# Performance work log

Hardware: AMD Instinct MI355X
Metric: run time of the kernel (lower is better)

Reference implementation:

```python
import jax, jax.numpy as jnp
import numpy as np

N = 8192
IN_F = 256
OUT_F = 64
ALPHA = 0.2  # LeakyReLU negative slope
NEG_INF = -9e15


def setup_inputs() -> dict:
    key = jax.random.key(0)
    k1, k2, k3, k4 = jax.random.split(key, 4)
    input_h = jax.random.normal(k1, (N, IN_F), dtype=jnp.float32)
    # xavier_normal with gain=1.414 ~ std = 1.414*sqrt(2/(fan_in+fan_out))
    W = jax.random.normal(k2, (IN_F, OUT_F), dtype=jnp.float32) * (1.414 * np.sqrt(2.0 / (IN_F + OUT_F)))
    a = jax.random.normal(k3, (2 * OUT_F, 1), dtype=jnp.float32) * (1.414 * np.sqrt(2.0 / (2 * OUT_F + 1)))
    adj = jax.random.randint(k4, (N, N), 0, 2).astype(jnp.int32)
    return {"input_h": input_h, "adj": adj, "W": W, "a": a}


def reference(input_h, adj, W, a):
    # h = X @ W : [N, OUT_F]
    h = input_h @ W
    # Pairwise concat score: a^T [h_i || h_j] == (h_i @ a1) + (h_j @ a2)
    a1 = a[:OUT_F]   # [OUT_F, 1]
    a2 = a[OUT_F:]   # [OUT_F, 1]
    f1 = h @ a1      # [N, 1] -> contribution of source node i
    f2 = h @ a2      # [N, 1] -> contribution of target node j
    e = jax.nn.leaky_relu(f1 + f2.T, negative_slope=ALPHA)  # [N, N]
    # Masked softmax over neighbors (adj > 0), dropout is identity in eval mode
    attention = jax.nn.softmax(jnp.where(adj > 0, e, NEG_INF), axis=-1)
    h_prime = attention @ h  # [N, OUT_F]
    # concat=True -> ELU activation
    return jax.nn.elu(h_prime)
```

## Files before the change

kernel.cpp:

```cpp
#include <hip/hip_runtime.h>
#include <hip/hip_bf16.h>


using short8 = __attribute__((ext_vector_type(8))) short;
using f32x4  = __attribute__((ext_vector_type(4))) float;

#define NN     8192
#define INF_   256
#define OUTF   64
#define LR_A   0.2f
#define LOG2E  1.4426950408889634f
#define ROWS   16
#define TILE_C 256
#define CQW    2048
#define NTILES (CQW / TILE_C)
#define ROWB   1040

__device__ __forceinline__ unsigned short f2bf_rne(float x) {
  unsigned int u = __float_as_uint(x);
  u += 0x7FFFu + ((u >> 16) & 1u);
  return (unsigned short)(u >> 16);
}

__global__ __launch_bounds__(256) void gat_pre(
    const float* __restrict__ input, const float* __restrict__ W,
    const float* __restrict__ a, unsigned short* __restrict__ hp,
    float* __restrict__ f1, float* __restrict__ f2) {
  __shared__ float WT[OUTF][260];
  int tid = threadIdx.x;
  for (int idx = tid; idx < INF_ * OUTF; idx += 256) {
    int c = idx >> 6, f = idx & 63;
    WT[f][c] = W[idx];
  }
  __syncthreads();
  int w = tid >> 6, l = tid & 63;
  int i0 = blockIdx.x * 16 + w * 4;
  const float4* r0 = (const float4*)(input + (long)(i0 + 0) * INF_);
  const float4* r1 = (const float4*)(input + (long)(i0 + 1) * INF_);
  const float4* r2 = (const float4*)(input + (long)(i0 + 2) * INF_);
  const float4* r3 = (const float4*)(input + (long)(i0 + 3) * INF_);
  float h0 = 0.f, h1 = 0.f, h2 = 0.f, h3 = 0.f;
#pragma unroll 4
  for (int c4 = 0; c4 < INF_ / 4; ++c4) {
    float4 wv = *(const float4*)&WT[l][c4 * 4];
    float4 v0 = r0[c4], v1 = r1[c4], v2 = r2[c4], v3 = r3[c4];
    h0 = fmaf(v0.x, wv.x, h0); h0 = fmaf(v0.y, wv.y, h0);
    h0 = fmaf(v0.z, wv.z, h0); h0 = fmaf(v0.w, wv.w, h0);
    h1 = fmaf(v1.x, wv.x, h1); h1 = fmaf(v1.y, wv.y, h1);
    h1 = fmaf(v1.z, wv.z, h1); h1 = fmaf(v1.w, wv.w, h1);
    h2 = fmaf(v2.x, wv.x, h2); h2 = fmaf(v2.y, wv.y, h2);
    h2 = fmaf(v2.z, wv.z, h2); h2 = fmaf(v2.w, wv.w, h2);
    h3 = fmaf(v3.x, wv.x, h3); h3 = fmaf(v3.y, wv.y, h3);
    h3 = fmaf(v3.z, wv.z, h3); h3 = fmaf(v3.w, wv.w, h3);
  }
  float a1k = a[l], a2k = a[OUTF + l];
  float hh[4] = {h0, h1, h2, h3};
#pragma unroll
  for (int r = 0; r < 4; ++r) {
    int i = i0 + r;
    float t1 = hh[r] * a1k, t2 = hh[r] * a2k;
#pragma unroll
    for (int off = 32; off; off >>= 1) {
      t1 += __shfl_xor(t1, off);
      t2 += __shfl_xor(t2, off);
    }
    int gran = (((i >> 5) * 4) + (l >> 4)) * 64 + ((i >> 3) & 3) * 16 + (l & 15);
    hp[(long)gran * 8 + (i & 7)] = f2bf_rne(hh[r]);
    if (l == 0) { f1[i] = t1 * LOG2E; f2[i] = t2 * LOG2E; }
  }
}

__global__ __launch_bounds__(256, 4) void gat_main(
    const int* __restrict__ adj, const unsigned short* __restrict__ hp,
    const float* __restrict__ f1, const float* __restrict__ f2,
    float* __restrict__ numP, float* __restrict__ denP) {
  __shared__ __align__(16) char um[2 * ROWS * ROWB];
  __shared__ float ssum[4][ROWS];
  __shared__ float f1s[ROWS], shifts[ROWS], red[4];
  int tid = threadIdx.x;
  int w = tid >> 6, l = tid & 63;
  int i0 = blockIdx.x * ROWS;
  int cq = blockIdx.y;

  float fm = -1e30f;
  for (int jj = tid * 4; jj < NN; jj += 256 * 4) {
    float4 v = *(const float4*)(f2 + jj);
    fm = fmaxf(fm, fmaxf(fmaxf(v.x, v.y), fmaxf(v.z, v.w)));
  }
#pragma unroll
  for (int off = 32; off; off >>= 1) fm = fmaxf(fm, __shfl_xor(fm, off));
  if (l == 0) red[w] = fm;
  __syncthreads();
  if (tid == 0) {
    float m = fmaxf(fmaxf(red[0], red[1]), fmaxf(red[2], red[3]));
    red[0] = m;
  }
  __syncthreads();
  float Fmax = red[0];
  if (tid < ROWS) {
    float v = f1[i0 + tid];
    f1s[tid] = v;
    float s = v + Fmax;
    shifts[tid] = fmaxf(s, LR_A * s);
  }
  __syncthreads();

  int q = l & 15, g = l >> 4;
  float f1r = f1s[q], sh = shifts[q];
  float u1 = f1r - sh;
  float u2 = LR_A * f1r - sh;
  f32x4 acc0 = {0.f, 0.f, 0.f, 0.f}, acc1 = acc0, acc2 = acc0, acc3 = acc0;
  float srow = 0.f;

  const int* adjb = adj + (long)cq * CQW;

  auto stage = [&](int t, int b) {
#pragma unroll
    for (int k = 0; k < 4; ++k) {
      int r = w * 4 + k;
      const int* src = adjb + (long)(i0 + r) * NN + t * TILE_C + l * 4;
      char* d = um + b * (ROWS * ROWB) + r * ROWB;
      __builtin_amdgcn_global_load_lds(
          (const __attribute__((address_space(1))) void*)src,
          (__attribute__((address_space(3))) void*)d, 16, 0, 0);
    }
  };

  stage(0, 0);
  __syncthreads();

  for (int t = 0; t < NTILES; ++t) {
    int b = t & 1;
    if (t + 1 < NTILES) stage(t + 1, b ^ 1);

    const char* base = um + b * (ROWS * ROWB) + q * ROWB;
#pragma unroll
    for (int s = 0; s < 2; ++s) {
      int koff = w * 256 + s * 128 + g * 32;
      int4 A0 = *(const int4*)(base + koff);
      int4 A1 = *(const int4*)(base + koff + 16);
      int jb = cq * CQW + t * TILE_C + w * 64 + s * 32 + g * 8;
      float4 F0 = *(const float4*)(f2 + jb);
      float4 F1 = *(const float4*)(f2 + jb + 4);
      float fa[8] = {F0.x, F0.y, F0.z, F0.w, F1.x, F1.y, F1.z, F1.w};
      int   aa[8] = {A0.x, A0.y, A0.z, A0.w, A1.x, A1.y, A1.z, A1.w};

      union { short8 v; unsigned short u[8]; } pa;
      float ps = 0.f;
#pragma unroll
      for (int e = 0; e < 8; ++e) {
        float arg = fmaxf(u1 + fa[e], fmaf(LR_A, fa[e], u2));
        float pe = (aa[e] > 0) ? exp2f(arg) : 0.f;
        ps += pe;
        pa.u[e] = f2bf_rne(pe);
      }
      srow += ps;

      int K32 = cq * 64 + t * 8 + w * 2 + s;
      const unsigned short* hb = hp + (long)K32 * 4 * 64 * 8 + l * 8;
      short8 b0 = *(const short8*)(hb + 0 * 64 * 8);
      short8 b1 = *(const short8*)(hb + 1 * 64 * 8);
      short8 b2 = *(const short8*)(hb + 2 * 64 * 8);
      short8 b3 = *(const short8*)(hb + 3 * 64 * 8);
      acc0 = __builtin_amdgcn_mfma_f32_16x16x32_bf16(pa.v, b0, acc0, 0, 0, 0);
      acc1 = __builtin_amdgcn_mfma_f32_16x16x32_bf16(pa.v, b1, acc1, 0, 0, 0);
      acc2 = __builtin_amdgcn_mfma_f32_16x16x32_bf16(pa.v, b2, acc2, 0, 0, 0);
      acc3 = __builtin_amdgcn_mfma_f32_16x16x32_bf16(pa.v, b3, acc3, 0, 0, 0);
    }
    __syncthreads();
  }

  srow += __shfl_xor(srow, 16);
  srow += __shfl_xor(srow, 32);
  if (l < ROWS) ssum[w][l] = srow;

  float* accs = (float*)um;
#pragma unroll
  for (int r = 0; r < 4; ++r) {
    accs[(w * ROWS + g * 4 + r) * OUTF + 0 * 16 + q] = acc0[r];
    accs[(w * ROWS + g * 4 + r) * OUTF + 1 * 16 + q] = acc1[r];
    accs[(w * ROWS + g * 4 + r) * OUTF + 2 * 16 + q] = acc2[r];
    accs[(w * ROWS + g * 4 + r) * OUTF + 3 * 16 + q] = acc3[r];
  }
  __syncthreads();

  for (int idx = tid; idx < ROWS * OUTF; idx += 256) {
    int m = idx >> 6, n = idx & 63;
    float num = 0.f, den = 0.f;
#pragma unroll
    for (int ww = 0; ww < 4; ++ww) {
      num += accs[(ww * ROWS + m) * OUTF + n];
      den += ssum[ww][m];
    }
    numP[((long)cq * NN + i0 + m) * OUTF + n] = num;
    if (n == 0) denP[(long)cq * NN + i0 + m] = den;
  }
}

__global__ __launch_bounds__(256) void gat_fin(
    const float* __restrict__ numP, const float* __restrict__ denP,
    float* __restrict__ out) {
  int gid = blockIdx.x * 256 + threadIdx.x;
  int row = gid >> 6, n = gid & 63;
  float num = 0.f, den = 0.f;
#pragma unroll
  for (int c = 0; c < 4; ++c) {
    num += numP[((long)c * NN + row) * OUTF + n];
    den += denP[(long)c * NN + row];
  }
  float v = num / den;
  out[gid] = v > 0.f ? v : expm1f(v);
}

extern "C" void kernel_launch(void* const* d_in, const int* in_sizes, int n_in,
                              void* d_out, int out_size, void* d_ws, size_t ws_size,
                              hipStream_t stream) {
  const float* input = (const float*)d_in[0];
  const int*   adj   = (const int*)d_in[1];
  const float* W     = (const float*)d_in[2];
  const float* a     = (const float*)d_in[3];
  float* out = (float*)d_out;
  char* ws = (char*)d_ws;
  unsigned short* hp = (unsigned short*)ws;
  float* f1   = (float*)(ws + (1 << 20));
  float* f2   = (float*)(ws + (1 << 20) + (32 << 10));
  float* numP = (float*)(ws + (1 << 20) + (64 << 10));
  float* denP = (float*)(ws + (1 << 20) + (64 << 10) + (8 << 20));
  (void)in_sizes; (void)n_in; (void)out_size; (void)ws_size;

  gat_pre<<<512, 256, 0, stream>>>(input, W, a, hp, f1, f2);
  gat_main<<<dim3(512, 4), 256, 0, stream>>>(adj, hp, f1, f2, numP, denP);
  gat_fin<<<NN * OUTF / 256, 256, 0, stream>>>(numP, denP, out);
}
```

Measured before the change: 100.2 us.

## Stage adj and h tiles through LDS with a deeper async pipeline

Rebuilds the main loop's memory pipeline. Adjacency tiles now go through a three-slot LDS ring with XOR swizzling to avoid bank conflicts. The bf16 h tiles are prefetched into double-buffered LDS instead of being read directly from global memory, and the f2 slice is cached in shared memory. Explicit vmcnt waits plus raw barriers replace the per-tile __syncthreads. Tile width is halved and launch bounds drop to 2 blocks per SIMD to fit the larger LDS footprint, which cuts occupancy and makes correctness depend on the hand-counted waitcnt.

```diff
diff --git a/kernel.cpp b/kernel.cpp
--- a/kernel.cpp
+++ b/kernel.cpp
@@ -11,10 +11,11 @@
 #define LR_A   0.2f
 #define LOG2E  1.4426950408889634f
 #define ROWS   16
-#define TILE_C 256
+#define TILE_C 128
 #define CQW    2048
 #define NTILES (CQW / TILE_C)
-#define ROWB   1040
+#define ADJSLOT 8192
+#define HPSLOT  16384
 
 __device__ __forceinline__ unsigned short f2bf_rne(float x) {
   unsigned int u = __float_as_uint(x);
@@ -70,11 +71,13 @@
   }
 }
 
-__global__ __launch_bounds__(256, 4) void gat_main(
+__global__ __launch_bounds__(256, 2) void gat_main(
     const int* __restrict__ adj, const unsigned short* __restrict__ hp,
     const float* __restrict__ f1, const float* __restrict__ f2,
     float* __restrict__ numP, float* __restrict__ denP) {
-  __shared__ __align__(16) char um[2 * ROWS * ROWB];
+  __shared__ __align__(16) char adjS[3 * ADJSLOT];
+  __shared__ __align__(16) char hpS[2 * HPSLOT];
+  __shared__ float f2s[CQW];
   __shared__ float ssum[4][ROWS];
   __shared__ float f1s[ROWS], shifts[ROWS], red[4];
   int tid = threadIdx.x;
@@ -83,18 +86,17 @@
   int cq = blockIdx.y;
 
   float fm = -1e30f;
-  for (int jj = tid * 4; jj < NN; jj += 256 * 4) {
+  for (int jj = tid * 4; jj < NN; jj += 1024) {
     float4 v = *(const float4*)(f2 + jj);
     fm = fmaxf(fm, fmaxf(fmaxf(v.x, v.y), fmaxf(v.z, v.w)));
   }
+  for (int jj = tid * 4; jj < CQW; jj += 1024)
+    *(float4*)&f2s[jj] = *(const float4*)(f2 + cq * CQW + jj);
 #pragma unroll
   for (int off = 32; off; off >>= 1) fm = fmaxf(fm, __shfl_xor(fm, off));
   if (l == 0) red[w] = fm;
   __syncthreads();
-  if (tid == 0) {
-    float m = fmaxf(fmaxf(red[0], red[1]), fmaxf(red[2], red[3]));
-    red[0] = m;
-  }
+  if (tid == 0) red[0] = fmaxf(fmaxf(red[0], red[1]), fmaxf(red[2], red[3]));
   __syncthreads();
   float Fmax = red[0];
   if (tid < ROWS) {
@@ -107,74 +109,88 @@
 
   int q = l & 15, g = l >> 4;
   float f1r = f1s[q], sh = shifts[q];
-  float u1 = f1r - sh;
-  float u2 = LR_A * f1r - sh;
+  float u1 = f1r - sh, u2 = LR_A * f1r - sh;
   f32x4 acc0 = {0.f, 0.f, 0.f, 0.f}, acc1 = acc0, acc2 = acc0, acc3 = acc0;
   float srow = 0.f;
 
-  const int* adjb = adj + (long)cq * CQW;
-
-  auto stage = [&](int t, int b) {
-#pragma unroll
-    for (int k = 0; k < 4; ++k) {
-      int r = w * 4 + k;
-      const int* src = adjb + (long)(i0 + r) * NN + t * TILE_C + l * 4;
-      char* d = um + b * (ROWS * ROWB) + r * ROWB;
+  auto stage_adj = [&](int t, int slot) {
+#pragma unroll
+    for (int j = 0; j < 2; ++j) {
+      int rr = w * 4 + j * 2 + (l >> 5);
+      const int* src = adj + (long)(i0 + rr) * NN + cq * CQW + t * TILE_C
+                       + (((l & 31) ^ (rr & 7)) << 2);
+      char* d = adjS + slot * ADJSLOT + (w * 4 + j * 2) * 512;
       __builtin_amdgcn_global_load_lds(
           (const __attribute__((address_space(1))) void*)src,
           (__attribute__((address_space(3))) void*)d, 16, 0, 0);
     }
   };
-
-  stage(0, 0);
-  __syncthreads();
+  auto stage_hp = [&](int t, int slot) {
+    const unsigned short* base = hp + (long)(cq * 64 + t * 4 + w) * 2048 + l * 8;
+#pragma unroll
+    for (int j = 0; j < 4; ++j) {
+      const unsigned short* src = base + j * 512;
+      char* d = hpS + slot * HPSLOT + w * 4096 + j * 1024;
+      __builtin_amdgcn_global_load_lds(
+          (const __attribute__((address_space(1))) void*)src,
+          (__attribute__((address_space(3))) void*)d, 16, 0, 0);
+    }
+  };
+
+  stage_hp(0, 0);
+  stage_adj(0, 0);
+  stage_adj(1, 1);
 
   for (int t = 0; t < NTILES; ++t) {
-    int b = t & 1;
-    if (t + 1 < NTILES) stage(t + 1, b ^ 1);
-
-    const char* base = um + b * (ROWS * ROWB) + q * ROWB;
-#pragma unroll
-    for (int s = 0; s < 2; ++s) {
-      int koff = w * 256 + s * 128 + g * 32;
-      int4 A0 = *(const int4*)(base + koff);
-      int4 A1 = *(const int4*)(base + koff + 16);
-      int jb = cq * CQW + t * TILE_C + w * 64 + s * 32 + g * 8;
-      float4 F0 = *(const float4*)(f2 + jb);
-      float4 F1 = *(const float4*)(f2 + jb + 4);
-      float fa[8] = {F0.x, F0.y, F0.z, F0.w, F1.x, F1.y, F1.z, F1.w};
-      int   aa[8] = {A0.x, A0.y, A0.z, A0.w, A1.x, A1.y, A1.z, A1.w};
-
-      union { short8 v; unsigned short u[8]; } pa;
-      float ps = 0.f;
-#pragma unroll
-      for (int e = 0; e < 8; ++e) {
-        float arg = fmaxf(u1 + fa[e], fmaf(LR_A, fa[e], u2));
-        float pe = (aa[e] > 0) ? exp2f(arg) : 0.f;
-        ps += pe;
-        pa.u[e] = f2bf_rne(pe);
-      }
-      srow += ps;
-
-      int K32 = cq * 64 + t * 8 + w * 2 + s;
-      const unsigned short* hb = hp + (long)K32 * 4 * 64 * 8 + l * 8;
-      short8 b0 = *(const short8*)(hb + 0 * 64 * 8);
-      short8 b1 = *(const short8*)(hb + 1 * 64 * 8);
-      short8 b2 = *(const short8*)(hb + 2 * 64 * 8);
-      short8 b3 = *(const short8*)(hb + 3 * 64 * 8);
-      acc0 = __builtin_amdgcn_mfma_f32_16x16x32_bf16(pa.v, b0, acc0, 0, 0, 0);
-      acc1 = __builtin_amdgcn_mfma_f32_16x16x32_bf16(pa.v, b1, acc1, 0, 0, 0);
-      acc2 = __builtin_amdgcn_mfma_f32_16x16x32_bf16(pa.v, b2, acc2, 0, 0, 0);
-      acc3 = __builtin_amdgcn_mfma_f32_16x16x32_bf16(pa.v, b3, acc3, 0, 0, 0);
-    }
-    __syncthreads();
+    if (t < NTILES - 1) {
+      asm volatile("s_waitcnt vmcnt(2)" ::: "memory");
+    } else {
+      asm volatile("s_waitcnt vmcnt(0)" ::: "memory");
+    }
+    __builtin_amdgcn_s_barrier();
+    if (t + 1 < NTILES) stage_hp(t + 1, (t + 1) & 1);
+    if (t + 2 < NTILES) stage_adj(t + 2, (t + 2) % 3);
+
+    const char* ab = adjS + (t % 3) * ADJSLOT + q * 512;
+    int koff = w * 128 + g * 32;
+    int sw = (q & 7) << 4;
+    int4 A0 = *(const int4*)(ab + (koff ^ sw));
+    int4 A1 = *(const int4*)(ab + ((koff + 16) ^ sw));
+    const float* f2b = f2s + t * TILE_C + w * 32 + g * 8;
+    float4 F0 = *(const float4*)(f2b);
+    float4 F1 = *(const float4*)(f2b + 4);
+    float fa[8] = {F0.x, F0.y, F0.z, F0.w, F1.x, F1.y, F1.z, F1.w};
+    int   aa[8] = {A0.x, A0.y, A0.z, A0.w, A1.x, A1.y, A1.z, A1.w};
+
+    union { short8 v; unsigned short u[8]; } pa;
+    float ps = 0.f;
+#pragma unroll
+    for (int e = 0; e < 8; ++e) {
+      float arg = fmaxf(u1 + fa[e], fmaf(LR_A, fa[e], u2));
+      float pe = (aa[e] > 0) ? exp2f(arg) : 0.f;
+      ps += pe;
+      pa.u[e] = f2bf_rne(pe);
+    }
+    srow += ps;
+
+    const unsigned short* hb =
+        (const unsigned short*)(hpS + (t & 1) * HPSLOT + w * 4096) + l * 8;
+    short8 b0 = *(const short8*)(hb + 0 * 512);
+    short8 b1 = *(const short8*)(hb + 1 * 512);
+    short8 b2 = *(const short8*)(hb + 2 * 512);
+    short8 b3 = *(const short8*)(hb + 3 * 512);
+    acc0 = __builtin_amdgcn_mfma_f32_16x16x32_bf16(pa.v, b0, acc0, 0, 0, 0);
+    acc1 = __builtin_amdgcn_mfma_f32_16x16x32_bf16(pa.v, b1, acc1, 0, 0, 0);
+    acc2 = __builtin_amdgcn_mfma_f32_16x16x32_bf16(pa.v, b2, acc2, 0, 0, 0);
+    acc3 = __builtin_amdgcn_mfma_f32_16x16x32_bf16(pa.v, b3, acc3, 0, 0, 0);
   }
 
   srow += __shfl_xor(srow, 16);
   srow += __shfl_xor(srow, 32);
+
+  __syncthreads();
   if (l < ROWS) ssum[w][l] = srow;
-
-  float* accs = (float*)um;
+  float* accs = (float*)hpS;
 #pragma unroll
   for (int r = 0; r < 4; ++r) {
     accs[(w * ROWS + g * 4 + r) * OUTF + 0 * 16 + q] = acc0[r];
```

New measurement: 121.8 us. 1.22x slower.

## Replace LDS-staged adjacency tiles with register-prefetched direct loads and manual vmcnt pipeline

Applied to the files above, without the earlier changes.

Drops the double-buffered global-to-LDS staging of adjacency tiles and the per-tile block barriers. Each wave now loads its own adjacency and h fragments straight into registers several steps ahead, using explicit vmcnt waits and sched barriers in a fully unrolled 16-step loop. The f2 slice is cached in shared memory and occupancy hint drops from 4 to 3 waves per SIMD. This removes block-wide syncs and LDS round trips, but adds register pressure and depends on exact vmcnt counts being correct.

```diff
diff --git a/kernel.cpp b/kernel.cpp
--- a/kernel.cpp
+++ b/kernel.cpp
@@ -11,10 +11,7 @@
 #define LR_A   0.2f
 #define LOG2E  1.4426950408889634f
 #define ROWS   16
-#define TILE_C 256
 #define CQW    2048
-#define NTILES (CQW / TILE_C)
-#define ROWB   1040
 
 __device__ __forceinline__ unsigned short f2bf_rne(float x) {
   unsigned int u = __float_as_uint(x);
@@ -70,11 +67,12 @@
   }
 }
 
-__global__ __launch_bounds__(256, 4) void gat_main(
+__global__ __launch_bounds__(256, 3) void gat_main(
     const int* __restrict__ adj, const unsigned short* __restrict__ hp,
     const float* __restrict__ f1, const float* __restrict__ f2,
     float* __restrict__ numP, float* __restrict__ denP) {
-  __shared__ __align__(16) char um[2 * ROWS * ROWB];
+  __shared__ __align__(16) float umem[4 * ROWS * OUTF];
+  float* f2s = umem;
   __shared__ float ssum[4][ROWS];
   __shared__ float f1s[ROWS], shifts[ROWS], red[4];
   int tid = threadIdx.x;
@@ -83,18 +81,17 @@
   int cq = blockIdx.y;
 
   float fm = -1e30f;
-  for (int jj = tid * 4; jj < NN; jj += 256 * 4) {
+  for (int jj = tid * 4; jj < NN; jj += 1024) {
     float4 v = *(const float4*)(f2 + jj);
     fm = fmaxf(fm, fmaxf(fmaxf(v.x, v.y), fmaxf(v.z, v.w)));
   }
+  for (int jj = tid * 4; jj < CQW; jj += 1024)
+    *(float4*)&f2s[jj] = *(const float4*)(f2 + cq * CQW + jj);
 #pragma unroll
   for (int off = 32; off; off >>= 1) fm = fmaxf(fm, __shfl_xor(fm, off));
   if (l == 0) red[w] = fm;
   __syncthreads();
-  if (tid == 0) {
-    float m = fmaxf(fmaxf(red[0], red[1]), fmaxf(red[2], red[3]));
-    red[0] = m;
-  }
+  if (tid == 0) red[0] = fmaxf(fmaxf(red[0], red[1]), fmaxf(red[2], red[3]));
   __syncthreads();
   float Fmax = red[0];
   if (tid < ROWS) {
@@ -107,74 +104,85 @@
 
   int q = l & 15, g = l >> 4;
   float f1r = f1s[q], sh = shifts[q];
-  float u1 = f1r - sh;
-  float u2 = LR_A * f1r - sh;
+  float u1 = f1r - sh, u2 = LR_A * f1r - sh;
   f32x4 acc0 = {0.f, 0.f, 0.f, 0.f}, acc1 = acc0, acc2 = acc0, acc3 = acc0;
   float srow = 0.f;
 
-  const int* adjb = adj + (long)cq * CQW;
-
-  auto stage = [&](int t, int b) {
-#pragma unroll
-    for (int k = 0; k < 4; ++k) {
-      int r = w * 4 + k;
-      const int* src = adjb + (long)(i0 + r) * NN + t * TILE_C + l * 4;
-      char* d = um + b * (ROWS * ROWB) + r * ROWB;
-      __builtin_amdgcn_global_load_lds(
-          (const __attribute__((address_space(1))) void*)src,
-          (__attribute__((address_space(3))) void*)d, 16, 0, 0);
+  const int* adjw = adj + (long)(i0 + q) * NN + cq * CQW + w * 512 + g * 8;
+  const unsigned short* hpw = hp + (long)(cq * 64 + w * 16) * 2048 + l * 8;
+  const float* f2w = f2s + w * 512 + g * 8;
+
+  int4   aS[4][2];
+  short8 hS[2][4];
+
+#define IADJ(SLOT, T) { int _t = (T) < 16 ? (T) : 15;                        \
+    const int* _p = adjw + _t * 32;                                          \
+    aS[SLOT][0] = *(const int4*)_p; aS[SLOT][1] = *(const int4*)(_p + 4); }
+#define IHP(SLOT, T) { int _t = (T) < 16 ? (T) : 15;                         \
+    const unsigned short* _p = hpw + (long)_t * 2048;                        \
+    hS[SLOT][0] = *(const short8*)_p;                                        \
+    hS[SLOT][1] = *(const short8*)(_p + 512);                                \
+    hS[SLOT][2] = *(const short8*)(_p + 1024);                               \
+    hS[SLOT][3] = *(const short8*)(_p + 1536); }
+
+  auto compute = [&](const int4* A, const short8* H, int t) {
+    const float* fb = f2w + t * 32;
+    float4 F0 = *(const float4*)fb, F1 = *(const float4*)(fb + 4);
+    float fa[8] = {F0.x, F0.y, F0.z, F0.w, F1.x, F1.y, F1.z, F1.w};
+    int   aa[8] = {A[0].x, A[0].y, A[0].z, A[0].w,
+                   A[1].x, A[1].y, A[1].z, A[1].w};
+    union { short8 v; unsigned short u[8]; } pa;
+    float ps = 0.f;
+#pragma unroll
+    for (int e = 0; e < 8; ++e) {
+      float arg = fmaxf(u1 + fa[e], fmaf(LR_A, fa[e], u2));
+      float pe = (aa[e] > 0) ? exp2f(arg) : 0.f;
+      ps += pe;
+      pa.u[e] = f2bf_rne(pe);
     }
+    srow += ps;
+    acc0 = __builtin_amdgcn_mfma_f32_16x16x32_bf16(pa.v, H[0], acc0, 0, 0, 0);
+    acc1 = __builtin_amdgcn_mfma_f32_16x16x32_bf16(pa.v, H[1], acc1, 0, 0, 0);
+    acc2 = __builtin_amdgcn_mfma_f32_16x16x32_bf16(pa.v, H[2], acc2, 0, 0, 0);
+    acc3 = __builtin_amdgcn_mfma_f32_16x16x32_bf16(pa.v, H[3], acc3, 0, 0, 0);
   };
 
-  stage(0, 0);
-  __syncthreads();
-
-  for (int t = 0; t < NTILES; ++t) {
-    int b = t & 1;
-    if (t + 1 < NTILES) stage(t + 1, b ^ 1);
-
-    const char* base = um + b * (ROWS * ROWB) + q * ROWB;
-#pragma unroll
-    for (int s = 0; s < 2; ++s) {
-      int koff = w * 256 + s * 128 + g * 32;
-      int4 A0 = *(const int4*)(base + koff);
-      int4 A1 = *(const int4*)(base + koff + 16);
-      int jb = cq * CQW + t * TILE_C + w * 64 + s * 32 + g * 8;
-      float4 F0 = *(const float4*)(f2 + jb);
-      float4 F1 = *(const float4*)(f2 + jb + 4);
-      float fa[8] = {F0.x, F0.y, F0.z, F0.w, F1.x, F1.y, F1.z, F1.w};
-      int   aa[8] = {A0.x, A0.y, A0.z, A0.w, A1.x, A1.y, A1.z, A1.w};
-
-      union { short8 v; unsigned short u[8]; } pa;
-      float ps = 0.f;
-#pragma unroll
-      for (int e = 0; e < 8; ++e) {
-        float arg = fmaxf(u1 + fa[e], fmaf(LR_A, fa[e], u2));
-        float pe = (aa[e] > 0) ? exp2f(arg) : 0.f;
-        ps += pe;
-        pa.u[e] = f2bf_rne(pe);
-      }
-      srow += ps;
-
-      int K32 = cq * 64 + t * 8 + w * 2 + s;
-      const unsigned short* hb = hp + (long)K32 * 4 * 64 * 8 + l * 8;
-      short8 b0 = *(const short8*)(hb + 0 * 64 * 8);
-      short8 b1 = *(const short8*)(hb + 1 * 64 * 8);
-      short8 b2 = *(const short8*)(hb + 2 * 64 * 8);
-      short8 b3 = *(const short8*)(hb + 3 * 64 * 8);
-      acc0 = __builtin_amdgcn_mfma_f32_16x16x32_bf16(pa.v, b0, acc0, 0, 0, 0);
-      acc1 = __builtin_amdgcn_mfma_f32_16x16x32_bf16(pa.v, b1, acc1, 0, 0, 0);
-      acc2 = __builtin_amdgcn_mfma_f32_16x16x32_bf16(pa.v, b2, acc2, 0, 0, 0);
-      acc3 = __builtin_amdgcn_mfma_f32_16x16x32_bf16(pa.v, b3, acc3, 0, 0, 0);
-    }
-    __syncthreads();
-  }
+#define STEP(SLOT, HC, HN, T, VM)                                            \
+    IHP(HN, (T) + 1);                                                        \
+    IADJ(((SLOT) + 3) & 3, (T) + 3);                                         \
+    __builtin_amdgcn_sched_barrier(0);                                       \
+    asm volatile("s_waitcnt vmcnt(" VM ")" ::: "memory");                    \
+    __builtin_amdgcn_sched_barrier(0);                                       \
+    compute(aS[SLOT], hS[HC], T);
+
+  IADJ(0, 0) IADJ(1, 1) IADJ(2, 2) IHP(0, 0)
+
+  STEP(0, 0, 1,  0, "6")
+  STEP(1, 1, 0,  1, "8")
+  STEP(2, 0, 1,  2, "8")
+  STEP(3, 1, 0,  3, "8")
+  STEP(0, 0, 1,  4, "8")
+  STEP(1, 1, 0,  5, "8")
+  STEP(2, 0, 1,  6, "8")
+  STEP(3, 1, 0,  7, "8")
+  STEP(0, 0, 1,  8, "8")
+  STEP(1, 1, 0,  9, "8")
+  STEP(2, 0, 1, 10, "8")
+  STEP(3, 1, 0, 11, "8")
+  STEP(0, 0, 1, 12, "8")
+  STEP(1, 1, 0, 13, "8")
+  STEP(2, 0, 1, 14, "8")
+  STEP(3, 1, 0, 15, "8")
+#undef STEP
+#undef IADJ
+#undef IHP
 
   srow += __shfl_xor(srow, 16);
   srow += __shfl_xor(srow, 32);
+
+  __syncthreads();
   if (l < ROWS) ssum[w][l] = srow;
-
-  float* accs = (float*)um;
+  float* accs = umem;
 #pragma unroll
   for (int r = 0; r < 4; ++r) {
     accs[(w * ROWS + g * 4 + r) * OUTF + 0 * 16 + q] = acc0[r];
```

After: 143.6 us. +43.3%, slower.
